# Kernel optimization log

Measured on AMD Instinct MI355X. Metric: run time of the kernel, lower is better.

Reference implementation:

```python
import jax, jax.numpy as jnp
import numpy as np
import math

B, S, D, H = 4, 2048, 512, 8
HD = D // H

def setup_inputs() -> dict:
    key = jax.random.key(0)
    ks = jax.random.split(key, 12)
    s_hd = 1.0 / math.sqrt(HD)
    s_d = 1.0 / math.sqrt(D)
    return {
        "q": jax.random.normal(ks[0], (B, S, D), jnp.float32),
        "k": jax.random.normal(ks[1], (B, S, D), jnp.float32),
        "v": jax.random.normal(ks[2], (B, S, D), jnp.float32),
        # torch nn.Linear(head_dim, head_dim): weight [HD, HD], bias [HD]
        "Wq": jax.random.uniform(ks[3], (HD, HD), jnp.float32, -s_hd, s_hd),
        "bq": jax.random.uniform(ks[4], (HD,), jnp.float32, -s_hd, s_hd),
        "Wk": jax.random.uniform(ks[5], (HD, HD), jnp.float32, -s_hd, s_hd),
        "bk": jax.random.uniform(ks[6], (HD,), jnp.float32, -s_hd, s_hd),
        "Wv": jax.random.uniform(ks[7], (HD, HD), jnp.float32, -s_hd, s_hd),
        "bv": jax.random.uniform(ks[8], (HD,), jnp.float32, -s_hd, s_hd),
        # output projection nn.Linear(d, d)
        "Wo": jax.random.uniform(ks[9], (D, D), jnp.float32, -s_d, s_d),
        "bo": jax.random.uniform(ks[10], (D,), jnp.float32, -s_d, s_d),
        # LayerNorm(d) affine params
        "gamma": jnp.ones((D,), jnp.float32),
        "beta": jnp.zeros((D,), jnp.float32),
    }

def _layernorm(x, gamma, beta, eps=1e-5):
    mu = jnp.mean(x, axis=-1, keepdims=True)
    var = jnp.var(x, axis=-1, keepdims=True)
    return (x - mu) * jax.lax.rsqrt(var + eps) * gamma + beta

def reference(q, k, v, Wq, bq, Wk, bk, Wv, bv, Wo, bo, gamma, beta):
    batch, q_len = q.shape[0], q.shape[1]
    # split heads: [B, L, H, HD]; per-head Linear shares one weight across heads
    Qh = q.reshape(batch, q_len, H, HD) @ Wq.T + bq
    Kh = k.reshape(batch, k.shape[1], H, HD) @ Wk.T + bk
    Vh = v.reshape(batch, v.shape[1], H, HD) @ Wv.T + bv
    # scores scaled by sqrt(d) (faithful to source, NOT sqrt(head_dim))
    scores = jnp.einsum('bqhd,bkhd->bhqk', Qh, Kh) / math.sqrt(D)
    attn = jax.nn.softmax(scores, axis=-1)
    out = jnp.einsum('bhqk,bkhd->bqhd', attn, Vh)
    concat = out.reshape(batch, q_len, D)
    lin = concat @ Wo.T + bo
    # AddNorm quirk: residual added AFTER LayerNorm (dropout = identity in eval)
    return q + _layernorm(lin, gamma, beta)
```

## Files before the change

kernel.cpp:

```cpp
#include <hip/hip_runtime.h>
#include <hip/hip_bf16.h>
#include <math.h>
#include <stdint.h>

#define B 4
#define S 2048
#define D 512
#define H 8
#define HD 64

typedef __attribute__((ext_vector_type(4))) int   int4v;
typedef __attribute__((ext_vector_type(8))) short short8;
typedef __attribute__((ext_vector_type(4))) short short4v;
typedef __attribute__((ext_vector_type(4))) float f32x4;

__device__ __forceinline__ unsigned short bfr(float x) {
    __bf16 h = (__bf16)x;
    union { __bf16 b; unsigned short s; } u; u.b = h; return u.s;
}
__device__ __forceinline__ float b2f(unsigned short s) {
    union { unsigned u; float f; } v; v.u = (unsigned)s << 16; return v.f;
}
__device__ __forceinline__ float ex2(float x) {
#if __has_builtin(__builtin_amdgcn_exp2f)
    return __builtin_amdgcn_exp2f(x);
#else
    return exp2f(x);
#endif
}
__device__ __forceinline__ short8 cvt8(const float* p) {
    float4 f0 = *(const float4*)p;
    float4 f1 = *(const float4*)(p + 4);
    short8 s8;
    s8[0] = (short)bfr(f0.x); s8[1] = (short)bfr(f0.y);
    s8[2] = (short)bfr(f0.z); s8[3] = (short)bfr(f0.w);
    s8[4] = (short)bfr(f1.x); s8[5] = (short)bfr(f1.y);
    s8[6] = (short)bfr(f1.z); s8[7] = (short)bfr(f1.w);
    return s8;
}

#define QSCALE 0.06377229601488305f
#define MFIX 4.0f

typedef const __attribute__((address_space(1))) unsigned char g8_t;
typedef __attribute__((address_space(3))) unsigned char l8_t;
__device__ __forceinline__ void gl_lds16(const unsigned short* g, unsigned short* l) {
#if __has_builtin(__builtin_amdgcn_global_load_lds)
    __builtin_amdgcn_global_load_lds((g8_t*)g, (l8_t*)l, 16, 0, 0);
#else
    int lane = threadIdx.x & 63;
    ((int4v*)l)[lane] = *(const int4v*)g;
#endif
}

__global__ __launch_bounds__(256) void qkv_mfma_kernel(
    const float* __restrict__ q, const float* __restrict__ k,
    const float* __restrict__ v,
    const float* __restrict__ Wq, const float* __restrict__ bq,
    const float* __restrict__ Wk, const float* __restrict__ bk,
    const float* __restrict__ Wv, const float* __restrict__ bv,
    const float* __restrict__ Wo, unsigned short* __restrict__ WoB,
    unsigned short* __restrict__ Qh, unsigned short* __restrict__ Kh,
    unsigned short* __restrict__ VtG)
{
    const int t = threadIdx.x;
    const int bid = blockIdx.x;
    if (bid >= 1536) {
        int i = (bid - 1536) * 1024 + t * 4;
        float4 f = *(const float4*)(Wo + i);
        short4v s;
        s[0] = (short)bfr(f.x); s[1] = (short)bfr(f.y);
        s[2] = (short)bfr(f.z); s[3] = (short)bfr(f.w);
        *(short4v*)(WoB + i) = s;
        return;
    }

    __shared__ __align__(16) unsigned short Wl[64 * 72];
    __shared__ __align__(16) unsigned short Tb[4][1536];

    const int x   = bid / 512;
    const int r_  = bid - x * 512;
    const int bh  = r_ >> 4;
    const int stg = r_ & 15;
    const int b = bh >> 3, h = bh & 7;
    const int L = t & 63, w = t >> 6;
    const int c = L & 15, qd = L >> 4;

    const float* Wf     = (x == 0) ? Wq : (x == 1) ? Wk : Wv;
    const float* bias_p = (x == 0) ? bq : (x == 1) ? bk : bv;
    const float* X      = (x == 0) ? q  : (x == 1) ? k  : v;

    unsigned short* Tw = Tb[w];

    {
        int row = t >> 2, col = (t & 3) * 16;
        *(short8*)&Wl[row * 72 + col]     = cvt8(Wf + t * 16);
        *(short8*)&Wl[row * 72 + col + 8] = cvt8(Wf + t * 16 + 8);
    }
    __syncthreads();

    short8 wf[4][2];
    #pragma unroll
    for (int nt = 0; nt < 4; ++nt)
        #pragma unroll
        for (int kc = 0; kc < 2; ++kc)
            wf[nt][kc] = *(const short8*)&Wl[(16 * nt + c) * 72 + kc * 32 + 8 * qd];

    if (x < 2) {
        float bias[4];
        #pragma unroll
        for (int nt = 0; nt < 4; ++nt) bias[nt] = bias_p[16 * nt + c];
        const float sc = (x == 0) ? QSCALE : 1.0f;
        #pragma unroll
        for (int ti = 0; ti < 2; ++ti) {
            const int st = stg * 8 + w * 2 + ti;
            const float* xrow = X + ((size_t)(b * S + st * 16 + c)) * D + h * HD;
            short8 af0 = cvt8(xrow + 8 * qd);
            short8 af1 = cvt8(xrow + 32 + 8 * qd);
            f32x4 acc[4];
            #pragma unroll
            for (int nt = 0; nt < 4; ++nt) {
                acc[nt] = (f32x4){bias[nt], bias[nt], bias[nt], bias[nt]};
                acc[nt] = __builtin_amdgcn_mfma_f32_16x16x32_bf16(af0, wf[nt][0], acc[nt], 0, 0, 0);
                acc[nt] = __builtin_amdgcn_mfma_f32_16x16x32_bf16(af1, wf[nt][1], acc[nt], 0, 0, 0);
            }
            #pragma unroll
            for (int nt = 0; nt < 4; ++nt)
                #pragma unroll
                for (int r = 0; r < 4; ++r)
                    Tw[(4 * qd + r) * 72 + 16 * nt + c] = bfr(acc[nt][r] * sc);
            int rw = L >> 2, cg_ = (L & 3) * 16;
            short8 s0 = *(const short8*)&Tw[rw * 72 + cg_];
            short8 s1 = *(const short8*)&Tw[rw * 72 + cg_ + 8];
            unsigned short* O = ((x == 0) ? Qh : Kh)
                              + ((size_t)(b * H + h) * S + st * 16) * HD;
            *(short8*)&O[rw * HD + cg_]     = s0;
            *(short8*)&O[rw * HD + cg_ + 8] = s1;
        }
    } else {
        f32x4 bias4[4];
        #pragma unroll
        for (int nt = 0; nt < 4; ++nt) {
            float4 bb4 = *(const float4*)(bias_p + 16 * nt + 4 * qd);
            bias4[nt] = (f32x4){bb4.x, bb4.y, bb4.z, bb4.w};
        }
        #pragma unroll
        for (int ti = 0; ti < 2; ++ti) {
            const int st = stg * 8 + w * 2 + ti;
            const float* xrow = X + ((size_t)(b * S + st * 16 + c)) * D + h * HD;
            short8 af0 = cvt8(xrow + 8 * qd);
            short8 af1 = cvt8(xrow + 32 + 8 * qd);
            f32x4 acc[4];
            #pragma unroll
            for (int nt = 0; nt < 4; ++nt) {
                acc[nt] = bias4[nt];
                acc[nt] = __builtin_amdgcn_mfma_f32_16x16x32_bf16(wf[nt][0], af0, acc[nt], 0, 0, 0);
                acc[nt] = __builtin_amdgcn_mfma_f32_16x16x32_bf16(wf[nt][1], af1, acc[nt], 0, 0, 0);
            }
            #pragma unroll
            for (int nt = 0; nt < 4; ++nt)
                #pragma unroll
                for (int r = 0; r < 4; ++r)
                    Tw[(16 * nt + 4 * qd + r) * 24 + c] = bfr(acc[nt][r]);
            short8 s0 = *(const short8*)&Tw[L * 24];
            short8 s1 = *(const short8*)&Tw[L * 24 + 8];
            unsigned short* O = VtG + (size_t)(b * H + h) * HD * S;
            *(short8*)&O[(size_t)L * S + st * 16]     = s0;
            *(short8*)&O[(size_t)L * S + st * 16 + 8] = s1;
        }
    }
}

__global__ __launch_bounds__(256, 4) void attn_kernel(
    const unsigned short* __restrict__ Qh, const unsigned short* __restrict__ Kh,
    const unsigned short* __restrict__ VtG, unsigned short* __restrict__ accPb,
    float* __restrict__ lP)
{
    __shared__ __align__(16) unsigned short Ks[2][4096];
    __shared__ __align__(16) unsigned short Vs[2][4096];

    const int idx = blockIdx.x;
    const int bh = idx & 31;
    const int rem = idx >> 5;
    const int qt = rem >> 1;
    const int ks = rem & 1;
    const int b = bh >> 3, h = bh & 7;
    const int t = threadIdx.x;
    const int w = t >> 6, L = t & 63;
    const int c = L & 15, qd = L >> 4;

    const unsigned short* Kb = Kh + ((size_t)bh * S + ks * 1024) * HD;
    const unsigned short* Vb = VtG + (size_t)bh * HD * S + ks * 1024;

    short8 qf[2][2];
    #pragma unroll
    for (int qg = 0; qg < 2; ++qg)
        #pragma unroll
        for (int kc = 0; kc < 2; ++kc)
            qf[qg][kc] = *(const short8*)(Qh
                + ((size_t)bh * S + qt * 128 + w * 32 + qg * 16 + c) * HD
                + kc * 32 + 8 * qd);

    f32x4 acc[2][4];
    f32x4 lacc[2];
    #pragma unroll
    for (int qg = 0; qg < 2; ++qg) {
        lacc[qg] = (f32x4){0.f, 0.f, 0.f, 0.f};
        #pragma unroll
        for (int dt = 0; dt < 4; ++dt) acc[qg][dt] = (f32x4){0.f, 0.f, 0.f, 0.f};
    }

    const short8 ones8 = {0x3F80, 0x3F80, 0x3F80, 0x3F80,
                          0x3F80, 0x3F80, 0x3F80, 0x3F80};

    const int sd = t >> 3, sj = t & 7;
    const int s3 = sj & 3;
    const int vslotp = sj >> 2;
    const int vadd = (s3 & 1) * 256 + (s3 >> 1) * 4;

    int4v vpre[2];
    #pragma unroll
    for (int i = 0; i < 2; ++i) {
        int bi = w + 4 * i;
        gl_lds16(Kb + (size_t)(16 * (bi >> 1) + c) * HD + (bi & 1) * 32 + qd * 8,
                 &Ks[0][bi * 512]);
        vpre[i] = *(const int4v*)(Vb + (size_t)(sd + 32 * i) * S + 8 * sj);
    }

    for (int it = 0; it < 16; ++it) {
        const int cur = it & 1, nxt = cur ^ 1;
        #pragma unroll
        for (int i = 0; i < 2; ++i) {
            int d = sd + 32 * i;
            int os = ((d >> 4) * 2 + vslotp) * 512 + (d & 15) * 8 + vadd;
            union { int4v v; short4v h[2]; } u; u.v = vpre[i];
            *(short4v*)&Vs[cur][os]       = u.h[0];
            *(short4v*)&Vs[cur][os + 128] = u.h[1];
        }
        __syncthreads();
        if (it + 1 < 16) {
            int n1 = (it + 1) * 64;
            #pragma unroll
            for (int i = 0; i < 2; ++i) {
                int bi = w + 4 * i;
                gl_lds16(Kb + (size_t)(n1 + 16 * (bi >> 1) + c) * HD + (bi & 1) * 32 + qd * 8,
                         &Ks[nxt][bi * 512]);
                vpre[i] = *(const int4v*)(Vb + (size_t)(sd + 32 * i) * S + n1 + 8 * sj);
            }
        }

        const unsigned short* KsC = Ks[cur];
        const unsigned short* VsC = Vs[cur];

        short8 ps[2][2];
        #pragma unroll
        for (int mt = 0; mt < 4; ++mt) {
            short8 a0 = *(const short8*)(KsC + (mt * 2 + 0) * 512 + L * 8);
            short8 a1 = *(const short8*)(KsC + (mt * 2 + 1) * 512 + L * 8);
            #pragma unroll
            for (int qg = 0; qg < 2; ++qg) {
                f32x4 stv = (f32x4){-MFIX, -MFIX, -MFIX, -MFIX};
                __builtin_amdgcn_s_setprio(1);
                stv = __builtin_amdgcn_mfma_f32_16x16x32_bf16(a0, qf[qg][0], stv, 0, 0, 0);
                stv = __builtin_amdgcn_mfma_f32_16x16x32_bf16(a1, qf[qg][1], stv, 0, 0, 0);
                __builtin_amdgcn_s_setprio(0);
                float p0 = ex2(stv[0]), p1 = ex2(stv[1]);
                float p2 = ex2(stv[2]), p3 = ex2(stv[3]);
                const int pp = mt >> 1, hl = (mt & 1) * 4;
                ps[qg][pp][hl + 0] = (short)bfr(p0);
                ps[qg][pp][hl + 1] = (short)bfr(p1);
                ps[qg][pp][hl + 2] = (short)bfr(p2);
                ps[qg][pp][hl + 3] = (short)bfr(p3);
            }
        }

        __builtin_amdgcn_s_setprio(1);
        #pragma unroll
        for (int pp = 0; pp < 2; ++pp) {
            lacc[0] = __builtin_amdgcn_mfma_f32_16x16x32_bf16(ps[0][pp], ones8, lacc[0], 0, 0, 0);
            lacc[1] = __builtin_amdgcn_mfma_f32_16x16x32_bf16(ps[1][pp], ones8, lacc[1], 0, 0, 0);
        }
        #pragma unroll
        for (int dt = 0; dt < 4; ++dt)
            #pragma unroll
            for (int pp = 0; pp < 2; ++pp) {
                short8 vb = *(const short8*)(VsC + (dt * 2 + pp) * 512 + L * 8);
                acc[0][dt] = __builtin_amdgcn_mfma_f32_16x16x32_bf16(ps[0][pp], vb, acc[0][dt], 0, 0, 0);
                acc[1][dt] = __builtin_amdgcn_mfma_f32_16x16x32_bf16(ps[1][pp], vb, acc[1][dt], 0, 0, 0);
            }
        __builtin_amdgcn_s_setprio(0);
    }

    const int q0 = qt * 128 + w * 32;
    unsigned short* accPp = accPb + (size_t)ks * ((size_t)B * S * D)
                          + ((size_t)b * S + q0) * D + h * HD;
    #pragma unroll
    for (int qg = 0; qg < 2; ++qg) {
        if (c == 0) {
            #pragma unroll
            for (int r = 0; r < 4; ++r)
                lP[(size_t)ks * ((size_t)B * H * S) + (size_t)bh * S
                   + q0 + qg * 16 + 4 * qd + r] = lacc[qg][r];
        }
        #pragma unroll
        for (int dt = 0; dt < 4; ++dt)
            #pragma unroll
            for (int r = 0; r < 4; ++r)
                accPp[(size_t)(qg * 16 + 4 * qd + r) * D + 16 * dt + c]
                    = bfr(acc[qg][dt][r]);
    }
}

__global__ __launch_bounds__(1024) void oproj_ln_kernel(
    const unsigned short* __restrict__ accPb, const float* __restrict__ lP,
    const unsigned short* __restrict__ WoB,
    const float* __restrict__ bo, const float* __restrict__ gamma,
    const float* __restrict__ beta, const float* __restrict__ qin,
    float* __restrict__ out)
{
    __shared__ __align__(16) unsigned short As[32 * 520];
    __shared__ float red[2][32][17];
    __shared__ float linv_s[32][8];
    __shared__ float mu_s2[32], rs_s2[32];

    const int t = threadIdx.x;
    const int r0 = blockIdx.x * 32;
    const int w = t >> 6, L = t & 63;
    const int c = L & 15, qd = L >> 4;
    const int n0 = w * 32;
    const size_t NEh = (size_t)B * S * D;
    const size_t BHS = (size_t)B * H * S;

    if (t < 256) {
        int row = t >> 3, hh = t & 7;
        int bb = r0 >> 11;
        int ss = (r0 & (S - 1)) + row;
        float l0 = lP[(size_t)(bb * H + hh) * S + ss];
        float l1 = lP[BHS + (size_t)(bb * H + hh) * S + ss];
        linv_s[row][hh] = 1.f / (l0 + l1);
    }
    __syncthreads();

    #pragma unroll
    for (int i = 0; i < 4; ++i) {
        int flat = t + 1024 * i;
        int row = flat >> 7, cg4 = flat & 127;
        int col = cg4 * 4;
        size_t gi = (size_t)(r0 + row) * D + col;
        short4v a0 = *(const short4v*)(accPb + gi);
        short4v a1 = *(const short4v*)(accPb + NEh + gi);
        float li = linv_s[row][col >> 6];
        short4v s;
        #pragma unroll
        for (int j = 0; j < 4; ++j)
            s[j] = (short)bfr((b2f((unsigned short)a0[j])
                             + b2f((unsigned short)a1[j])) * li);
        *(short4v*)&As[row * 520 + col] = s;
    }
    __syncthreads();

    f32x4 acc[2][2];
    #pragma unroll
    for (int nt = 0; nt < 2; ++nt) {
        float bv_ = bo[n0 + 16 * nt + c];
        acc[0][nt] = (f32x4){bv_, bv_, bv_, bv_};
        acc[1][nt] = (f32x4){bv_, bv_, bv_, bv_};
    }

    for (int kc = 0; kc < 16; ++kc) {
        short8 a0 = *(const short8*)&As[c * 520 + kc * 32 + 8 * qd];
        short8 a1 = *(const short8*)&As[(16 + c) * 520 + kc * 32 + 8 * qd];
        #pragma unroll
        for (int nt = 0; nt < 2; ++nt) {
            short8 bf = *(const short8*)(WoB + (size_t)(n0 + 16 * nt + c) * D
                                         + kc * 32 + 8 * qd);
            acc[0][nt] = __builtin_amdgcn_mfma_f32_16x16x32_bf16(a0, bf, acc[0][nt], 0, 0, 0);
            acc[1][nt] = __builtin_amdgcn_mfma_f32_16x16x32_bf16(a1, bf, acc[1][nt], 0, 0, 0);
        }
    }

    float sm[2][4], sq[2][4];
    #pragma unroll
    for (int mt = 0; mt < 2; ++mt)
        #pragma unroll
        for (int r = 0; r < 4; ++r) { sm[mt][r] = 0.f; sq[mt][r] = 0.f; }
    #pragma unroll
    for (int mt = 0; mt < 2; ++mt)
        #pragma unroll
        for (int nt = 0; nt < 2; ++nt)
            #pragma unroll
            for (int r = 0; r < 4; ++r) {
                float x_ = acc[mt][nt][r];
                sm[mt][r] += x_; sq[mt][r] += x_ * x_;
            }
    #pragma unroll
    for (int mask = 1; mask <= 8; mask <<= 1)
        #pragma unroll
        for (int mt = 0; mt < 2; ++mt)
            #pragma unroll
            for (int r = 0; r < 4; ++r) {
                sm[mt][r] += __shfl_xor(sm[mt][r], mask);
                sq[mt][r] += __shfl_xor(sq[mt][r], mask);
            }
    if (c == 0) {
        #pragma unroll
        for (int mt = 0; mt < 2; ++mt)
            #pragma unroll
            for (int r = 0; r < 4; ++r) {
                red[0][mt * 16 + 4 * qd + r][w] = sm[mt][r];
                red[1][mt * 16 + 4 * qd + r][w] = sq[mt][r];
            }
    }
    __syncthreads();

    if (t < 32) {
        float s_ = 0.f, q_ = 0.f;
        #pragma unroll
        for (int w_ = 0; w_ < 16; ++w_) { s_ += red[0][t][w_]; q_ += red[1][t][w_]; }
        float mu_ = s_ * (1.f / D);
        float var = q_ * (1.f / D) - mu_ * mu_;
        mu_s2[t] = mu_;
        rs_s2[t] = rsqrtf(var + 1e-5f);
    }
    __syncthreads();

    #pragma unroll
    for (int nt = 0; nt < 2; ++nt) {
        int n = n0 + 16 * nt + c;
        float g = gamma[n], be = beta[n];
        #pragma unroll
        for (int mt = 0; mt < 2; ++mt)
            #pragma unroll
            for (int r = 0; r < 4; ++r) {
                int m = mt * 16 + 4 * qd + r;
                size_t gi = (size_t)(r0 + m) * D + n;
                out[gi] = qin[gi] + (acc[mt][nt][r] - mu_s2[m]) * rs_s2[m] * g + be;
            }
    }
}

extern "C" void kernel_launch(void* const* d_in, const int* in_sizes, int n_in,
                              void* d_out, int out_size, void* d_ws, size_t ws_size,
                              hipStream_t stream) {
    const float* q     = (const float*)d_in[0];
    const float* k     = (const float*)d_in[1];
    const float* v     = (const float*)d_in[2];
    const float* Wq    = (const float*)d_in[3];
    const float* bq    = (const float*)d_in[4];
    const float* Wk    = (const float*)d_in[5];
    const float* bk    = (const float*)d_in[6];
    const float* Wv    = (const float*)d_in[7];
    const float* bv    = (const float*)d_in[8];
    const float* Wo    = (const float*)d_in[9];
    const float* bo    = (const float*)d_in[10];
    const float* gamma = (const float*)d_in[11];
    const float* beta  = (const float*)d_in[12];
    float* out = (float*)d_out;

    const size_t NE = (size_t)B * S * D;
    unsigned short* wsu = (unsigned short*)d_ws;
    unsigned short* Qh    = wsu;
    unsigned short* Kh    = wsu + NE;
    unsigned short* VtG   = wsu + 2 * NE;
    unsigned short* WoB   = wsu + 3 * NE;
    unsigned short* accPb = WoB + (size_t)D * D;
    float* lP = (float*)(accPb + 2 * NE);

    hipLaunchKernelGGL(qkv_mfma_kernel, dim3(1536 + 256), dim3(256), 0, stream,
                       q, k, v, Wq, bq, Wk, bk, Wv, bv, Wo, WoB, Qh, Kh, VtG);
    hipLaunchKernelGGL(attn_kernel, dim3(1024), dim3(256), 0, stream,
                       Qh, Kh, VtG, accPb, lP);
    hipLaunchKernelGGL(oproj_ln_kernel, dim3(B * S / 32), dim3(1024), 0, stream,
                       accPb, lP, WoB, bo, gamma, beta, q, out);
}
```

Before: 180.7 us.

## Halve attention query tile and read V directly from global memory

The attention kernel now gives each wave 16 query rows instead of 32, doubling the grid to 2048 blocks and raising the launch-bounds occupancy target to 8 blocks per CU. The shared-memory staging of V is removed, so V fragments are loaded straight from global memory as two 4-element reads per MFMA operand. This cuts register and LDS pressure so more waves can hide latency. In exchange, each K tile is reused by half as many queries, and the V reads become uncached, narrower global loads repeated per block.

```diff
diff --git a/kernel.cpp b/kernel.cpp
--- a/kernel.cpp
+++ b/kernel.cpp
@@ -171,13 +171,12 @@
     }
 }
 
-__global__ __launch_bounds__(256, 4) void attn_kernel(
+__global__ __launch_bounds__(256, 8) void attn_kernel(
     const unsigned short* __restrict__ Qh, const unsigned short* __restrict__ Kh,
     const unsigned short* __restrict__ VtG, unsigned short* __restrict__ accPb,
     float* __restrict__ lP)
 {
     __shared__ __align__(16) unsigned short Ks[2][4096];
-    __shared__ __align__(16) unsigned short Vs[2][4096];
 
     const int idx = blockIdx.x;
     const int bh = idx & 31;
@@ -192,51 +191,34 @@
     const unsigned short* Kb = Kh + ((size_t)bh * S + ks * 1024) * HD;
     const unsigned short* Vb = VtG + (size_t)bh * HD * S + ks * 1024;
 
-    short8 qf[2][2];
-    #pragma unroll
-    for (int qg = 0; qg < 2; ++qg)
-        #pragma unroll
-        for (int kc = 0; kc < 2; ++kc)
-            qf[qg][kc] = *(const short8*)(Qh
-                + ((size_t)bh * S + qt * 128 + w * 32 + qg * 16 + c) * HD
-                + kc * 32 + 8 * qd);
-
-    f32x4 acc[2][4];
-    f32x4 lacc[2];
-    #pragma unroll
-    for (int qg = 0; qg < 2; ++qg) {
-        lacc[qg] = (f32x4){0.f, 0.f, 0.f, 0.f};
-        #pragma unroll
-        for (int dt = 0; dt < 4; ++dt) acc[qg][dt] = (f32x4){0.f, 0.f, 0.f, 0.f};
-    }
+    short8 qf[2];
+    #pragma unroll
+    for (int kc = 0; kc < 2; ++kc)
+        qf[kc] = *(const short8*)(Qh
+            + ((size_t)bh * S + qt * 64 + w * 16 + c) * HD + kc * 32 + 8 * qd);
+
+    f32x4 acc[4];
+    f32x4 lacc = (f32x4){0.f, 0.f, 0.f, 0.f};
+    #pragma unroll
+    for (int dt = 0; dt < 4; ++dt) acc[dt] = (f32x4){0.f, 0.f, 0.f, 0.f};
 
     const short8 ones8 = {0x3F80, 0x3F80, 0x3F80, 0x3F80,
                           0x3F80, 0x3F80, 0x3F80, 0x3F80};
 
-    const int sd = t >> 3, sj = t & 7;
-    const int s3 = sj & 3;
-    const int vslotp = sj >> 2;
-    const int vadd = (s3 & 1) * 256 + (s3 >> 1) * 4;
-
-    int4v vpre[2];
+    const unsigned short* vrow[4];
+    #pragma unroll
+    for (int dt = 0; dt < 4; ++dt)
+        vrow[dt] = Vb + (size_t)(16 * dt + c) * S + 4 * qd;
+
     #pragma unroll
     for (int i = 0; i < 2; ++i) {
         int bi = w + 4 * i;
         gl_lds16(Kb + (size_t)(16 * (bi >> 1) + c) * HD + (bi & 1) * 32 + qd * 8,
                  &Ks[0][bi * 512]);
-        vpre[i] = *(const int4v*)(Vb + (size_t)(sd + 32 * i) * S + 8 * sj);
     }
 
     for (int it = 0; it < 16; ++it) {
-        const int cur = it & 1, nxt = cur ^ 1;
-        #pragma unroll
-        for (int i = 0; i < 2; ++i) {
-            int d = sd + 32 * i;
-            int os = ((d >> 4) * 2 + vslotp) * 512 + (d & 15) * 8 + vadd;
-            union { int4v v; short4v h[2]; } u; u.v = vpre[i];
-            *(short4v*)&Vs[cur][os]       = u.h[0];
-            *(short4v*)&Vs[cur][os + 128] = u.h[1];
-        }
+        const int cur = it & 1;
         __syncthreads();
         if (it + 1 < 16) {
             int n1 = (it + 1) * 64;
@@ -244,71 +226,60 @@
             for (int i = 0; i < 2; ++i) {
                 int bi = w + 4 * i;
                 gl_lds16(Kb + (size_t)(n1 + 16 * (bi >> 1) + c) * HD + (bi & 1) * 32 + qd * 8,
-                         &Ks[nxt][bi * 512]);
-                vpre[i] = *(const int4v*)(Vb + (size_t)(sd + 32 * i) * S + n1 + 8 * sj);
-            }
-        }
-
+                         &Ks[cur ^ 1][bi * 512]);
+            }
+        }
+        const int n0 = it * 64;
         const unsigned short* KsC = Ks[cur];
-        const unsigned short* VsC = Vs[cur];
-
-        short8 ps[2][2];
+
+        short8 ps[2];
         #pragma unroll
         for (int mt = 0; mt < 4; ++mt) {
             short8 a0 = *(const short8*)(KsC + (mt * 2 + 0) * 512 + L * 8);
             short8 a1 = *(const short8*)(KsC + (mt * 2 + 1) * 512 + L * 8);
-            #pragma unroll
-            for (int qg = 0; qg < 2; ++qg) {
-                f32x4 stv = (f32x4){-MFIX, -MFIX, -MFIX, -MFIX};
-                __builtin_amdgcn_s_setprio(1);
-                stv = __builtin_amdgcn_mfma_f32_16x16x32_bf16(a0, qf[qg][0], stv, 0, 0, 0);
-                stv = __builtin_amdgcn_mfma_f32_16x16x32_bf16(a1, qf[qg][1], stv, 0, 0, 0);
-                __builtin_amdgcn_s_setprio(0);
-                float p0 = ex2(stv[0]), p1 = ex2(stv[1]);
-                float p2 = ex2(stv[2]), p3 = ex2(stv[3]);
-                const int pp = mt >> 1, hl = (mt & 1) * 4;
-                ps[qg][pp][hl + 0] = (short)bfr(p0);
-                ps[qg][pp][hl + 1] = (short)bfr(p1);
-                ps[qg][pp][hl + 2] = (short)bfr(p2);
-                ps[qg][pp][hl + 3] = (short)bfr(p3);
-            }
+            f32x4 stv = (f32x4){-MFIX, -MFIX, -MFIX, -MFIX};
+            __builtin_amdgcn_s_setprio(1);
+            stv = __builtin_amdgcn_mfma_f32_16x16x32_bf16(a0, qf[0], stv, 0, 0, 0);
+            stv = __builtin_amdgcn_mfma_f32_16x16x32_bf16(a1, qf[1], stv, 0, 0, 0);
+            __builtin_amdgcn_s_setprio(0);
+            float p0 = ex2(stv[0]), p1 = ex2(stv[1]);
+            float p2 = ex2(stv[2]), p3 = ex2(stv[3]);
+            const int pp = mt >> 1, hl = (mt & 1) * 4;
+            ps[pp][hl + 0] = (short)bfr(p0);
+            ps[pp][hl + 1] = (short)bfr(p1);
+            ps[pp][hl + 2] = (short)bfr(p2);
+            ps[pp][hl + 3] = (short)bfr(p3);
         }
 
         __builtin_amdgcn_s_setprio(1);
-        #pragma unroll
-        for (int pp = 0; pp < 2; ++pp) {
-            lacc[0] = __builtin_amdgcn_mfma_f32_16x16x32_bf16(ps[0][pp], ones8, lacc[0], 0, 0, 0);
-            lacc[1] = __builtin_amdgcn_mfma_f32_16x16x32_bf16(ps[1][pp], ones8, lacc[1], 0, 0, 0);
-        }
+        lacc = __builtin_amdgcn_mfma_f32_16x16x32_bf16(ps[0], ones8, lacc, 0, 0, 0);
+        lacc = __builtin_amdgcn_mfma_f32_16x16x32_bf16(ps[1], ones8, lacc, 0, 0, 0);
         #pragma unroll
         for (int dt = 0; dt < 4; ++dt)
             #pragma unroll
             for (int pp = 0; pp < 2; ++pp) {
-                short8 vb = *(const short8*)(VsC + (dt * 2 + pp) * 512 + L * 8);
-                acc[0][dt] = __builtin_amdgcn_mfma_f32_16x16x32_bf16(ps[0][pp], vb, acc[0][dt], 0, 0, 0);
-                acc[1][dt] = __builtin_amdgcn_mfma_f32_16x16x32_bf16(ps[1][pp], vb, acc[1][dt], 0, 0, 0);
+                union { short8 v8; short4v h[2]; } u;
+                u.h[0] = *(const short4v*)(vrow[dt] + n0 + pp * 32);
+                u.h[1] = *(const short4v*)(vrow[dt] + n0 + pp * 32 + 16);
+                acc[dt] = __builtin_amdgcn_mfma_f32_16x16x32_bf16(ps[pp], u.v8, acc[dt], 0, 0, 0);
             }
         __builtin_amdgcn_s_setprio(0);
     }
 
-    const int q0 = qt * 128 + w * 32;
+    const int q0 = qt * 64 + w * 16;
     unsigned short* accPp = accPb + (size_t)ks * ((size_t)B * S * D)
                           + ((size_t)b * S + q0) * D + h * HD;
-    #pragma unroll
-    for (int qg = 0; qg < 2; ++qg) {
-        if (c == 0) {
-            #pragma unroll
-            for (int r = 0; r < 4; ++r)
-                lP[(size_t)ks * ((size_t)B * H * S) + (size_t)bh * S
-                   + q0 + qg * 16 + 4 * qd + r] = lacc[qg][r];
-        }
-        #pragma unroll
-        for (int dt = 0; dt < 4; ++dt)
-            #pragma unroll
-            for (int r = 0; r < 4; ++r)
-                accPp[(size_t)(qg * 16 + 4 * qd + r) * D + 16 * dt + c]
-                    = bfr(acc[qg][dt][r]);
-    }
+    if (c == 0) {
+        #pragma unroll
+        for (int r = 0; r < 4; ++r)
+            lP[(size_t)ks * ((size_t)B * H * S) + (size_t)bh * S
+               + q0 + 4 * qd + r] = lacc[r];
+    }
+    #pragma unroll
+    for (int dt = 0; dt < 4; ++dt)
+        #pragma unroll
+        for (int r = 0; r < 4; ++r)
+            accPp[(size_t)(4 * qd + r) * D + 16 * dt + c] = bfr(acc[dt][r]);
 }
 
 __global__ __launch_bounds__(1024) void oproj_ln_kernel(
@@ -468,7 +439,7 @@
 
     hipLaunchKernelGGL(qkv_mfma_kernel, dim3(1536 + 256), dim3(256), 0, stream,
                        q, k, v, Wq, bq, Wk, bk, Wv, bv, Wo, WoB, Qh, Kh, VtG);
-    hipLaunchKernelGGL(attn_kernel, dim3(1024), dim3(256), 0, stream,
+    hipLaunchKernelGGL(attn_kernel, dim3(2048), dim3(256), 0, stream,
                        Qh, Kh, VtG, accPb, lP);
     hipLaunchKernelGGL(oproj_ln_kernel, dim3(B * S / 32), dim3(1024), 0, stream,
                        accPb, lP, WoB, bo, gamma, beta, q, out);
```

Result: slower. 401.7 us (+122.3%).

## Shrink oproj row tile to 16 and load QKV weights directly

Applied to the files above, without the earlier changes.

The output-projection/LayerNorm kernel now handles 16 rows per block with 512 threads, each wave covering 64 output columns, so there are twice as many blocks. This should improve occupancy and SM fill, at the cost of reading the Wo weights twice as often overall. Separately, the QKV kernel drops its LDS staging and __syncthreads for the 64x64 head weight and reads the MFMA fragments straight from global memory. That removes a barrier but adds redundant global reads.

```diff
diff --git a/kernel.cpp b/kernel.cpp
--- a/kernel.cpp
+++ b/kernel.cpp
@@ -75,7 +75,6 @@
         return;
     }
 
-    __shared__ __align__(16) unsigned short Wl[64 * 72];
     __shared__ __align__(16) unsigned short Tb[4][1536];
 
     const int x   = bid / 512;
@@ -92,19 +91,12 @@
 
     unsigned short* Tw = Tb[w];
 
-    {
-        int row = t >> 2, col = (t & 3) * 16;
-        *(short8*)&Wl[row * 72 + col]     = cvt8(Wf + t * 16);
-        *(short8*)&Wl[row * 72 + col + 8] = cvt8(Wf + t * 16 + 8);
-    }
-    __syncthreads();
-
     short8 wf[4][2];
     #pragma unroll
     for (int nt = 0; nt < 4; ++nt)
         #pragma unroll
         for (int kc = 0; kc < 2; ++kc)
-            wf[nt][kc] = *(const short8*)&Wl[(16 * nt + c) * 72 + kc * 32 + 8 * qd];
+            wf[nt][kc] = cvt8(Wf + (16 * nt + c) * HD + kc * 32 + 8 * qd);
 
     if (x < 2) {
         float bias[4];
@@ -311,27 +303,27 @@
     }
 }
 
-__global__ __launch_bounds__(1024) void oproj_ln_kernel(
+__global__ __launch_bounds__(512) void oproj_ln_kernel(
     const unsigned short* __restrict__ accPb, const float* __restrict__ lP,
     const unsigned short* __restrict__ WoB,
     const float* __restrict__ bo, const float* __restrict__ gamma,
     const float* __restrict__ beta, const float* __restrict__ qin,
     float* __restrict__ out)
 {
-    __shared__ __align__(16) unsigned short As[32 * 520];
-    __shared__ float red[2][32][17];
-    __shared__ float linv_s[32][8];
-    __shared__ float mu_s2[32], rs_s2[32];
+    __shared__ __align__(16) unsigned short As[16 * 520];
+    __shared__ float red[2][16][9];
+    __shared__ float linv_s[16][8];
+    __shared__ float mu_s2[16], rs_s2[16];
 
     const int t = threadIdx.x;
-    const int r0 = blockIdx.x * 32;
+    const int r0 = blockIdx.x * 16;
     const int w = t >> 6, L = t & 63;
     const int c = L & 15, qd = L >> 4;
-    const int n0 = w * 32;
+    const int n0 = w * 64;
     const size_t NEh = (size_t)B * S * D;
     const size_t BHS = (size_t)B * H * S;
 
-    if (t < 256) {
+    if (t < 128) {
         int row = t >> 3, hh = t & 7;
         int bb = r0 >> 11;
         int ss = (r0 & (S - 1)) + row;
@@ -343,7 +335,7 @@
 
     #pragma unroll
     for (int i = 0; i < 4; ++i) {
-        int flat = t + 1024 * i;
+        int flat = t + 512 * i;
         int row = flat >> 7, cg4 = flat & 127;
         int col = cg4 * 4;
         size_t gi = (size_t)(r0 + row) * D + col;
@@ -359,64 +351,53 @@
     }
     __syncthreads();
 
-    f32x4 acc[2][2];
-    #pragma unroll
-    for (int nt = 0; nt < 2; ++nt) {
+    f32x4 acc[4];
+    #pragma unroll
+    for (int nt = 0; nt < 4; ++nt) {
         float bv_ = bo[n0 + 16 * nt + c];
-        acc[0][nt] = (f32x4){bv_, bv_, bv_, bv_};
-        acc[1][nt] = (f32x4){bv_, bv_, bv_, bv_};
+        acc[nt] = (f32x4){bv_, bv_, bv_, bv_};
     }
 
     for (int kc = 0; kc < 16; ++kc) {
         short8 a0 = *(const short8*)&As[c * 520 + kc * 32 + 8 * qd];
-        short8 a1 = *(const short8*)&As[(16 + c) * 520 + kc * 32 + 8 * qd];
-        #pragma unroll
-        for (int nt = 0; nt < 2; ++nt) {
+        #pragma unroll
+        for (int nt = 0; nt < 4; ++nt) {
             short8 bf = *(const short8*)(WoB + (size_t)(n0 + 16 * nt + c) * D
                                          + kc * 32 + 8 * qd);
-            acc[0][nt] = __builtin_amdgcn_mfma_f32_16x16x32_bf16(a0, bf, acc[0][nt], 0, 0, 0);
-            acc[1][nt] = __builtin_amdgcn_mfma_f32_16x16x32_bf16(a1, bf, acc[1][nt], 0, 0, 0);
-        }
-    }
-
-    float sm[2][4], sq[2][4];
-    #pragma unroll
-    for (int mt = 0; mt < 2; ++mt)
-        #pragma unroll
-        for (int r = 0; r < 4; ++r) { sm[mt][r] = 0.f; sq[mt][r] = 0.f; }
-    #pragma unroll
-    for (int mt = 0; mt < 2; ++mt)
-        #pragma unroll
-        for (int nt = 0; nt < 2; ++nt)
-            #pragma unroll
-            for (int r = 0; r < 4; ++r) {
-                float x_ = acc[mt][nt][r];
-                sm[mt][r] += x_; sq[mt][r] += x_ * x_;
-            }
+            acc[nt] = __builtin_amdgcn_mfma_f32_16x16x32_bf16(a0, bf, acc[nt], 0, 0, 0);
+        }
+    }
+
+    float sm[4], sq[4];
+    #pragma unroll
+    for (int r = 0; r < 4; ++r) { sm[r] = 0.f; sq[r] = 0.f; }
+    #pragma unroll
+    for (int nt = 0; nt < 4; ++nt)
+        #pragma unroll
+        for (int r = 0; r < 4; ++r) {
+            float x_ = acc[nt][r];
+            sm[r] += x_; sq[r] += x_ * x_;
+        }
     #pragma unroll
     for (int mask = 1; mask <= 8; mask <<= 1)
         #pragma unroll
-        for (int mt = 0; mt < 2; ++mt)
-            #pragma unroll
-            for (int r = 0; r < 4; ++r) {
-                sm[mt][r] += __shfl_xor(sm[mt][r], mask);
-                sq[mt][r] += __shfl_xor(sq[mt][r], mask);
-            }
+        for (int r = 0; r < 4; ++r) {
+            sm[r] += __shfl_xor(sm[r], mask);
+            sq[r] += __shfl_xor(sq[r], mask);
+        }
     if (c == 0) {
         #pragma unroll
-        for (int mt = 0; mt < 2; ++mt)
-            #pragma unroll
-            for (int r = 0; r < 4; ++r) {
-                red[0][mt * 16 + 4 * qd + r][w] = sm[mt][r];
-                red[1][mt * 16 + 4 * qd + r][w] = sq[mt][r];
-            }
+        for (int r = 0; r < 4; ++r) {
+            red[0][4 * qd + r][w] = sm[r];
+            red[1][4 * qd + r][w] = sq[r];
+        }
     }
     __syncthreads();
 
-    if (t < 32) {
+    if (t < 16) {
         float s_ = 0.f, q_ = 0.f;
         #pragma unroll
-        for (int w_ = 0; w_ < 16; ++w_) { s_ += red[0][t][w_]; q_ += red[1][t][w_]; }
+        for (int w_ = 0; w_ < 8; ++w_) { s_ += red[0][t][w_]; q_ += red[1][t][w_]; }
         float mu_ = s_ * (1.f / D);
         float var = q_ * (1.f / D) - mu_ * mu_;
         mu_s2[t] = mu_;
@@ -425,17 +406,15 @@
     __syncthreads();
 
     #pragma unroll
-    for (int nt = 0; nt < 2; ++nt) {
+    for (int nt = 0; nt < 4; ++nt) {
         int n = n0 + 16 * nt + c;
         float g = gamma[n], be = beta[n];
         #pragma unroll
-        for (int mt = 0; mt < 2; ++mt)
-            #pragma unroll
-            for (int r = 0; r < 4; ++r) {
-                int m = mt * 16 + 4 * qd + r;
-                size_t gi = (size_t)(r0 + m) * D + n;
-                out[gi] = qin[gi] + (acc[mt][nt][r] - mu_s2[m]) * rs_s2[m] * g + be;
-            }
+        for (int r = 0; r < 4; ++r) {
+            int m = 4 * qd + r;
+            size_t gi = (size_t)(r0 + m) * D + n;
+            out[gi] = qin[gi] + (acc[nt][r] - mu_s2[m]) * rs_s2[m] * g + be;
+        }
     }
 }
 
@@ -470,6 +449,6 @@
                        q, k, v, Wq, bq, Wk, bk, Wv, bv, Wo, WoB, Qh, Kh, VtG);
     hipLaunchKernelGGL(attn_kernel, dim3(1024), dim3(256), 0, stream,
                        Qh, Kh, VtG, accPb, lP);
-    hipLaunchKernelGGL(oproj_ln_kernel, dim3(B * S / 32), dim3(1024), 0, stream,
+    hipLaunchKernelGGL(oproj_ln_kernel, dim3(B * S / 16), dim3(512), 0, stream,
                        accPb, lP, WoB, bo, gamma, beta, q, out);
 }
```

After: 198.7 us. 10.0% more time.

## Split attention keys four ways and combine partials with float atomics

Applied to the files above, without the earlier changes.

The attention kernel now splits each key sequence into four chunks instead of two, doubling the grid to 2048 blocks. The per-split bf16 partial outputs and separate row sums are replaced by float atomicAdd into one zeroed accumulator buffer. The output-projection kernel then reads a single float partial instead of summing two bf16 partials. This raises parallelism and drops the separate combine buffers, at the cost of a memset, heavy atomic traffic (4x4 blocks per row region) and nondeterministic summation order.

```diff
diff --git a/kernel.cpp b/kernel.cpp
--- a/kernel.cpp
+++ b/kernel.cpp
@@ -173,7 +173,7 @@
 
 __global__ __launch_bounds__(256, 4) void attn_kernel(
     const unsigned short* __restrict__ Qh, const unsigned short* __restrict__ Kh,
-    const unsigned short* __restrict__ VtG, unsigned short* __restrict__ accPb,
+    const unsigned short* __restrict__ VtG, float* __restrict__ accP,
     float* __restrict__ lP)
 {
     __shared__ __align__(16) unsigned short Ks[2][4096];
@@ -182,15 +182,15 @@
     const int idx = blockIdx.x;
     const int bh = idx & 31;
     const int rem = idx >> 5;
-    const int qt = rem >> 1;
-    const int ks = rem & 1;
+    const int qt = rem >> 2;
+    const int ks = rem & 3;
     const int b = bh >> 3, h = bh & 7;
     const int t = threadIdx.x;
     const int w = t >> 6, L = t & 63;
     const int c = L & 15, qd = L >> 4;
 
-    const unsigned short* Kb = Kh + ((size_t)bh * S + ks * 1024) * HD;
-    const unsigned short* Vb = VtG + (size_t)bh * HD * S + ks * 1024;
+    const unsigned short* Kb = Kh + ((size_t)bh * S + ks * 512) * HD;
+    const unsigned short* Vb = VtG + (size_t)bh * HD * S + ks * 512;
 
     short8 qf[2][2];
     #pragma unroll
@@ -227,7 +227,7 @@
         vpre[i] = *(const int4v*)(Vb + (size_t)(sd + 32 * i) * S + 8 * sj);
     }
 
-    for (int it = 0; it < 16; ++it) {
+    for (int it = 0; it < 8; ++it) {
         const int cur = it & 1, nxt = cur ^ 1;
         #pragma unroll
         for (int i = 0; i < 2; ++i) {
@@ -238,7 +238,7 @@
             *(short4v*)&Vs[cur][os + 128] = u.h[1];
         }
         __syncthreads();
-        if (it + 1 < 16) {
+        if (it + 1 < 8) {
             int n1 = (it + 1) * 64;
             #pragma unroll
             for (int i = 0; i < 2; ++i) {
@@ -292,27 +292,26 @@
     }
 
     const int q0 = qt * 128 + w * 32;
-    unsigned short* accPp = accPb + (size_t)ks * ((size_t)B * S * D)
-                          + ((size_t)b * S + q0) * D + h * HD;
+    float* accPp = accP + ((size_t)b * S + q0) * D + h * HD;
     #pragma unroll
     for (int qg = 0; qg < 2; ++qg) {
         if (c == 0) {
             #pragma unroll
             for (int r = 0; r < 4; ++r)
-                lP[(size_t)ks * ((size_t)B * H * S) + (size_t)bh * S
-                   + q0 + qg * 16 + 4 * qd + r] = lacc[qg][r];
+                atomicAdd(&lP[(size_t)bh * S + q0 + qg * 16 + 4 * qd + r],
+                          lacc[qg][r]);
         }
         #pragma unroll
         for (int dt = 0; dt < 4; ++dt)
             #pragma unroll
             for (int r = 0; r < 4; ++r)
-                accPp[(size_t)(qg * 16 + 4 * qd + r) * D + 16 * dt + c]
-                    = bfr(acc[qg][dt][r]);
+                atomicAdd(&accPp[(size_t)(qg * 16 + 4 * qd + r) * D + 16 * dt + c],
+                          acc[qg][dt][r]);
     }
 }
 
 __global__ __launch_bounds__(1024) void oproj_ln_kernel(
-    const unsigned short* __restrict__ accPb, const float* __restrict__ lP,
+    const float* __restrict__ accP, const float* __restrict__ lP,
     const unsigned short* __restrict__ WoB,
     const float* __restrict__ bo, const float* __restrict__ gamma,
     const float* __restrict__ beta, const float* __restrict__ qin,
@@ -328,16 +327,12 @@
     const int w = t >> 6, L = t & 63;
     const int c = L & 15, qd = L >> 4;
     const int n0 = w * 32;
-    const size_t NEh = (size_t)B * S * D;
-    const size_t BHS = (size_t)B * H * S;
 
     if (t < 256) {
         int row = t >> 3, hh = t & 7;
         int bb = r0 >> 11;
         int ss = (r0 & (S - 1)) + row;
-        float l0 = lP[(size_t)(bb * H + hh) * S + ss];
-        float l1 = lP[BHS + (size_t)(bb * H + hh) * S + ss];
-        linv_s[row][hh] = 1.f / (l0 + l1);
+        linv_s[row][hh] = 1.f / lP[(size_t)(bb * H + hh) * S + ss];
     }
     __syncthreads();
 
@@ -347,14 +342,13 @@
         int row = flat >> 7, cg4 = flat & 127;
         int col = cg4 * 4;
         size_t gi = (size_t)(r0 + row) * D + col;
-        short4v a0 = *(const short4v*)(accPb + gi);
-        short4v a1 = *(const short4v*)(accPb + NEh + gi);
+        float4 a = *(const float4*)(accP + gi);
         float li = linv_s[row][col >> 6];
         short4v s;
-        #pragma unroll
-        for (int j = 0; j < 4; ++j)
-            s[j] = (short)bfr((b2f((unsigned short)a0[j])
-                             + b2f((unsigned short)a1[j])) * li);
+        s[0] = (short)bfr(a.x * li);
+        s[1] = (short)bfr(a.y * li);
+        s[2] = (short)bfr(a.z * li);
+        s[3] = (short)bfr(a.w * li);
         *(short4v*)&As[row * 520 + col] = s;
     }
     __syncthreads();
@@ -458,18 +452,21 @@
     float* out = (float*)d_out;
 
     const size_t NE = (size_t)B * S * D;
+    const size_t BHS = (size_t)B * H * S;
     unsigned short* wsu = (unsigned short*)d_ws;
     unsigned short* Qh    = wsu;
     unsigned short* Kh    = wsu + NE;
     unsigned short* VtG   = wsu + 2 * NE;
     unsigned short* WoB   = wsu + 3 * NE;
-    unsigned short* accPb = WoB + (size_t)D * D;
-    float* lP = (float*)(accPb + 2 * NE);
+    float* accP = (float*)(WoB + (size_t)D * D);
+    float* lP   = accP + NE;
+
+    hipMemsetAsync(accP, 0, (NE + BHS) * sizeof(float), stream);
 
     hipLaunchKernelGGL(qkv_mfma_kernel, dim3(1536 + 256), dim3(256), 0, stream,
                        q, k, v, Wq, bq, Wk, bk, Wv, bv, Wo, WoB, Qh, Kh, VtG);
-    hipLaunchKernelGGL(attn_kernel, dim3(1024), dim3(256), 0, stream,
-                       Qh, Kh, VtG, accPb, lP);
+    hipLaunchKernelGGL(attn_kernel, dim3(2048), dim3(256), 0, stream,
+                       Qh, Kh, VtG, accP, lP);
     hipLaunchKernelGGL(oproj_ln_kernel, dim3(B * S / 32), dim3(1024), 0, stream,
-                       accPb, lP, WoB, bo, gamma, beta, q, out);
-}
+                       accP, lP, WoB, bo, gamma, beta, q, out);
+}
```

Result: slower. 227.0 us (+25.6%).
